# Kernel optimization log

Measured on AMD Instinct MI355X. Metric: run time of the kernel, lower is better.

The kernel has to match this reference:

```python
import jax, jax.numpy as jnp
import numpy as np

B, S, DIM = 2, 2048, 2048
N_HEADS, N_KV_HEADS = 16, 4
HEAD_DIM = DIM // N_HEADS  # 128
N_REP = N_HEADS // N_KV_HEADS
ROPE_THETA = 10000.0


def _rope_cos_sin(bsz, seqlen, head_dim, theta):
    # precompute_freqs_cis (unscaled): angles[t, i] = t * theta^{-2i/d}
    inv_freq = 1.0 / (theta ** (np.arange(0, head_dim, 2)[: head_dim // 2].astype(np.float32) / head_dim))
    t = np.arange(seqlen, dtype=np.float32)
    ang = np.outer(t, inv_freq)  # [S, hd/2]
    cos = np.broadcast_to(np.cos(ang), (bsz, seqlen, head_dim // 2))
    sin = np.broadcast_to(np.sin(ang), (bsz, seqlen, head_dim // 2))
    return jnp.asarray(cos), jnp.asarray(sin)


def setup_inputs() -> dict:
    key = jax.random.key(0)
    ks = jax.random.split(key, 5)
    scale = 1.0 / np.sqrt(DIM)
    x = jax.random.normal(ks[0], (B, S, DIM), dtype=jnp.float32)
    wq = jax.random.normal(ks[1], (DIM, N_HEADS * HEAD_DIM), dtype=jnp.float32) * scale
    wk = jax.random.normal(ks[2], (DIM, N_KV_HEADS * HEAD_DIM), dtype=jnp.float32) * scale
    wv = jax.random.normal(ks[3], (DIM, N_KV_HEADS * HEAD_DIM), dtype=jnp.float32) * scale
    wo = jax.random.normal(ks[4], (N_HEADS * HEAD_DIM, DIM), dtype=jnp.float32) * scale
    freqs_cos, freqs_sin = _rope_cos_sin(B, S, HEAD_DIM, ROPE_THETA)
    return {"x": x, "wq": wq, "wk": wk, "wv": wv, "wo": wo,
            "freqs_cos": freqs_cos, "freqs_sin": freqs_sin}


def _apply_rope(t, cos, sin):
    # t: [B, S, H, hd]; cos/sin: [B, S, hd/2] -> complex mult on (even, odd) pairs
    tr = t.reshape(*t.shape[:-1], -1, 2)  # [B,S,H,hd/2,2]
    xr, xi = tr[..., 0], tr[..., 1]
    c = cos[:, :, None, :]
    s = sin[:, :, None, :]
    out_r = xr * c - xi * s
    out_i = xr * s + xi * c
    return jnp.stack([out_r, out_i], axis=-1).reshape(t.shape)


def reference(x, wq, wk, wv, wo, freqs_cos, freqs_sin):
    bsz, seqlen, _ = x.shape
    xq = (x @ wq).reshape(bsz, seqlen, N_HEADS, HEAD_DIM)
    xk = (x @ wk).reshape(bsz, seqlen, N_KV_HEADS, HEAD_DIM)
    xv = (x @ wv).reshape(bsz, seqlen, N_KV_HEADS, HEAD_DIM)

    xq = _apply_rope(xq, freqs_cos, freqs_sin)
    xk = _apply_rope(xk, freqs_cos, freqs_sin)

    # repeat_kv (GQA): [B,S,KV,hd] -> [B,S,H,hd]
    xk = jnp.repeat(xk, N_REP, axis=2)
    xv = jnp.repeat(xv, N_REP, axis=2)

    # [B,H,Sq,Sk]
    scores = jnp.einsum('bqhd,bkhd->bhqk', xq, xk) / np.sqrt(HEAD_DIM).astype(np.float32)
    # additive causal mask (triu of -inf, diagonal=1)
    causal = jnp.triu(jnp.full((seqlen, seqlen), -jnp.inf, dtype=scores.dtype), k=1)
    scores = scores + causal
    probs = jax.nn.softmax(scores.astype(jnp.float32), axis=-1).astype(xq.dtype)
    out = jnp.einsum('bhqk,bkhd->bqhd', probs, xv).reshape(bsz, seqlen, -1)
    return out @ wo
```

## Files before the change

kernel.cpp:

```cpp
#include <hip/hip_runtime.h>
#include <stdint.h>

#define SEQ   2048
#define NB    2
#define LDQKV 3072
#define HD    128
#define QSCALE2 (0.08838834764831845f * 1.44269504088896340f)

typedef __attribute__((ext_vector_type(8))) short short8;
typedef __attribute__((ext_vector_type(4))) short short4v;
typedef __attribute__((ext_vector_type(4))) float f32x4;
typedef __attribute__((ext_vector_type(16))) float f32x16;
typedef __attribute__((ext_vector_type(4))) unsigned int u32x4;
typedef __attribute__((ext_vector_type(2))) unsigned int u32x2;
typedef __attribute__((ext_vector_type(8))) __bf16 bf16x8;

__device__ __forceinline__ float bs2f(short s) {
  unsigned int u = ((unsigned int)(unsigned short)s) << 16;
  return __builtin_bit_cast(float, u);
}
__device__ __forceinline__ short f2bs(float f) {
  unsigned int u = __builtin_bit_cast(unsigned int, f);
  u += 0x7fffu + ((u >> 16) & 1u);
  return (short)(u >> 16);
}
__device__ __forceinline__ unsigned int cvt_pk(float lo, float hi) {
  unsigned int r;
  asm("v_cvt_pk_bf16_f32 %0, %1, %2" : "=v"(r) : "v"(lo), "v"(hi));
  return r;
}
__device__ __forceinline__ f32x4 mfma16(short8 a, short8 b, f32x4 c) {
  return __builtin_amdgcn_mfma_f32_16x16x32_bf16(
      __builtin_bit_cast(bf16x8, a), __builtin_bit_cast(bf16x8, b), c, 0, 0, 0);
}
__device__ __forceinline__ f32x16 mfma32(short8 a, short8 b, f32x16 c) {
  return __builtin_amdgcn_mfma_f32_32x32x16_bf16(
      __builtin_bit_cast(bf16x8, a), __builtin_bit_cast(bf16x8, b), c, 0, 0, 0);
}
__device__ __forceinline__ void gload_lds16(const void* g, void* l) {
  __builtin_amdgcn_global_load_lds(
      (__attribute__((address_space(1))) const void*)(uintptr_t)g,
      (__attribute__((address_space(3))) void*)(unsigned int)(uintptr_t)l,
      16, 0, 0);
}

#define SBAR() asm volatile("s_barrier" ::: "memory")
#define VMC(n) asm volatile("s_waitcnt vmcnt(" #n ")" ::: "memory")

__global__ __launch_bounds__(256) void k_prep(const float* __restrict__ x,
                                              const float* __restrict__ wq,
                                              const float* __restrict__ wk,
                                              const float* __restrict__ wv,
                                              const float* __restrict__ wo,
                                              short* __restrict__ xb,
                                              short* __restrict__ wT,
                                              short* __restrict__ woT) {
  __shared__ __align__(16) float tile[64][68];
  const int bid = blockIdx.x, t = threadIdx.x;
  if (bid < 4096) {
    int i = bid * 256 + t;
    f32x4 a = *(const f32x4*)(x + (size_t)i * 8);
    f32x4 b = *(const f32x4*)(x + (size_t)i * 8 + 4);
    short8 o;
#pragma unroll
    for (int j = 0; j < 4; ++j) { o[j] = f2bs(a[j]); o[4 + j] = f2bs(b[j]); }
    *(short8*)(xb + (size_t)i * 8) = o;
    return;
  }
  const float* src;
  short* dst;
  int N, id;
  if (bid < 5120)      { id = bid - 4096; src = wq; dst = wT;                        N = 2048; }
  else if (bid < 5376) { id = bid - 5120; src = wk; dst = wT + (size_t)2048 * 2048;  N = 512;  }
  else if (bid < 5632) { id = bid - 5376; src = wv; dst = wT + (size_t)2560 * 2048;  N = 512;  }
  else                 { id = bid - 5632; src = wo; dst = woT;                       N = 2048; }
  const int K = 2048;
  int k0 = (id & 31) * 64, n0 = (id >> 5) * 64;
#pragma unroll
  for (int rep = 0; rep < 4; ++rep) {
    int lin = rep * 1024 + t * 4;
    int kk = lin >> 6, nn = lin & 63;
    f32x4 v = *(const f32x4*)(src + (size_t)(k0 + kk) * N + n0 + nn);
    *(f32x4*)(&tile[kk][nn]) = v;
  }
  __syncthreads();
#pragma unroll
  for (int rep = 0; rep < 4; ++rep) {
    int lin = rep * 1024 + t * 4;
    int nn = lin >> 6, kk = lin & 63;
    short4v o;
#pragma unroll
    for (int j = 0; j < 4; ++j) o[j] = f2bs(tile[kk + j][nn]);
    *(short4v*)(dst + (size_t)(n0 + nn) * K + k0 + kk) = o;
  }
}

template <int NH, int FP32OUT>
__global__ __launch_bounds__(512, 2) void k_gemm256(const short* __restrict__ A,
                                                    const short* __restrict__ Bt,
                                                    void* __restrict__ Cp,
                                                    int M, int N, int K) {
  __shared__ short Al[2][2][128 * 64];
  __shared__ short Bl[2][NH][128 * 64];
  const int t = threadIdx.x, l = t & 63, w = t >> 6;
  const int pm = w >> 2, pn = w & 3;
  const int lrow = l & 15, lg = l >> 4;
  const int NT = K >> 6;

  const int nbm = M >> 8;
  const int per = gridDim.x >> 3;
  const int id2 = (blockIdx.x & 7) * per + (blockIdx.x >> 3);
  const int m0 = (id2 % nbm) * 256, n0 = (id2 / nbm) * (NH * 128);

  const int srow = w * 8 + (l >> 3);
  const int sgx = ((l & 7) ^ (srow & 7)) * 8;
  const short* Abase = A + (size_t)(m0 + srow) * K + sgx;
  const short* Bbase = Bt + (size_t)(n0 + srow) * K + sgx;

  f32x4 acc[8][NH * 2] = {};
  short8 aFr0[4][2], aFr1[4][2], bFr[NH][2][2];

  auto stgA = [&](int d, int h, int tv) {
    const short* g = Abase + (size_t)(h * 128) * K + (size_t)tv * 64;
    gload_lds16(g, &Al[d][h][w * 512]);
    gload_lds16(g + (size_t)64 * K, &Al[d][h][w * 512 + 4096]);
  };
  auto stgB = [&](int d, int h, int tv) {
    const short* g = Bbase + (size_t)(h * 128) * K + (size_t)tv * 64;
    gload_lds16(g, &Bl[d][h][w * 512]);
    gload_lds16(g + (size_t)64 * K, &Bl[d][h][w * 512 + 4096]);
  };
  auto rdA = [&](int d, int Mh, short8 (*dst)[2]) {
#pragma unroll
    for (int mi = 0; mi < 4; ++mi) {
      int rl = pm * 64 + mi * 16 + lrow;
#pragma unroll
      for (int kk = 0; kk < 2; ++kk)
        dst[mi][kk] = *(const short8*)&Al[d][Mh][rl * 64 +
                                                 (((kk * 4 + lg) ^ (rl & 7)) * 8)];
    }
  };
  auto rdB = [&](int d) {
#pragma unroll
    for (int h = 0; h < NH; ++h)
#pragma unroll
      for (int ni = 0; ni < 2; ++ni) {
        int rl = pn * 32 + ni * 16 + lrow;
#pragma unroll
        for (int kk = 0; kk < 2; ++kk)
          bFr[h][ni][kk] =
              *(const short8*)&Bl[d][h][rl * 64 +
                                        (((kk * 4 + lg) ^ (rl & 7)) * 8)];
      }
  };

#define MMH(Mh, FR)                                                          \
  do {                                                                       \
    __builtin_amdgcn_s_setprio(1);                                           \
    _Pragma("unroll") for (int h = 0; h < NH; ++h)                           \
        _Pragma("unroll") for (int mi = 0; mi < 4; ++mi)                     \
            _Pragma("unroll") for (int ni = 0; ni < 2; ++ni)                 \
                _Pragma("unroll") for (int kk = 0; kk < 2; ++kk)             \
                    acc[(Mh)*4 + mi][h * 2 + ni] =                           \
                        mfma16(FR[mi][kk], bFr[h][ni][kk],                   \
                               acc[(Mh)*4 + mi][h * 2 + ni]);                \
    __builtin_amdgcn_s_setprio(0);                                           \
  } while (0)

  stgA(0, 0, 0);
  for (int h = 0; h < NH; ++h) stgB(0, h, 0);
  stgA(0, 1, 0);
  stgA(1, 0, 1);
  if (NH == 2) stgB(1, 1, 1);
  if (NH == 2) { VMC(4); } else { VMC(2); }
  SBAR();

  for (int v = 0; v < NT; ++v) {
    const int d = v & 1, d1 = d ^ 1;
    rdA(d, 0, aFr0);
    rdB(d);
    rdA(d, 1, aFr1);
    if (v + 1 < NT) { stgB(d1, 0, v + 1); stgA(d1, 1, v + 1); }
    MMH(0, aFr0);
    SBAR();
    if (v + 2 < NT) {
      stgA(d, 0, v + 2);
      if (NH == 2) stgB(d, 1, v + 2);
    }
    MMH(1, aFr1);
    if (v + 2 < NT) {
      if (NH == 2) { VMC(4); } else { VMC(2); }
    } else {
      VMC(0);
    }
    SBAR();
  }
#undef MMH

#pragma unroll
  for (int Mh = 0; Mh < 2; ++Mh)
#pragma unroll
    for (int mi = 0; mi < 4; ++mi)
#pragma unroll
      for (int h = 0; h < NH; ++h)
#pragma unroll
        for (int ni = 0; ni < 2; ++ni) {
          int row = m0 + Mh * 128 + pm * 64 + mi * 16 + lg * 4;
          int col = n0 + h * 128 + pn * 32 + ni * 16 + lrow;
          f32x4 vv = acc[Mh * 4 + mi][h * 2 + ni];
#pragma unroll
          for (int v2 = 0; v2 < 4; ++v2) {
            if constexpr (FP32OUT)
              ((float*)Cp)[(size_t)(row + v2) * N + col] = vv[v2];
            else
              ((short*)Cp)[(size_t)(row + v2) * N + col] = f2bs(vv[v2]);
          }
        }
}

__global__ __launch_bounds__(256) void k_rv(short* __restrict__ qkv,
                                            const float* __restrict__ fcos,
                                            const float* __restrict__ fsin,
                                            short* __restrict__ vt) {
  __shared__ short tile[128 * 137];
  const int bid = blockIdx.x, t = threadIdx.x;
  if (bid < 5120) {
    int tid = bid * 256 + t;
    int p16 = tid & 15;
    int slice = (tid >> 4) % 20;
    int bs = tid / 320;
    int col = (slice < 16) ? slice * 128 + p16 * 8
                           : 2048 + (slice - 16) * 128 + p16 * 8;
    short8 x = *(short8*)(qkv + (size_t)bs * LDQKV + col);
    f32x4 c = *(const f32x4*)(fcos + (size_t)bs * 64 + p16 * 4);
    f32x4 s = *(const f32x4*)(fsin + (size_t)bs * 64 + p16 * 4);
    float sc = (slice < 16) ? QSCALE2 : 1.0f;
    short8 o;
#pragma unroll
    for (int j = 0; j < 4; ++j) {
      float xr = bs2f(x[2 * j]), xi = bs2f(x[2 * j + 1]);
      o[2 * j] = f2bs((xr * c[j] - xi * s[j]) * sc);
      o[2 * j + 1] = f2bs((xr * s[j] + xi * c[j]) * sc);
    }
    *(short8*)(qkv + (size_t)bs * LDQKV + col) = o;
    return;
  }
  const int id = bid - 5120;
  int s0 = (id & 15) * 128;
  int kvh = (id >> 4) & 3, b = id >> 6;
  const short* src = qkv + (size_t)(b * SEQ) * LDQKV + 2560 + kvh * 128;
#pragma unroll
  for (int rep = 0; rep < 8; ++rep) {
    int lin = rep * 2048 + t * 8;
    int si = lin >> 7, d = lin & 127;
    short8 v = *(const short8*)(src + (size_t)(s0 + si) * LDQKV + d);
#pragma unroll
    for (int j = 0; j < 8; ++j) tile[si * 137 + d + j] = v[j];
  }
  __syncthreads();
  short* dst = vt + (size_t)((b * 4 + kvh) * 128) * SEQ;
#pragma unroll
  for (int rep = 0; rep < 8; ++rep) {
    int lin = rep * 2048 + t * 8;
    int d = lin >> 7, sb = lin & 127;
    short8 o;
#pragma unroll
    for (int j = 0; j < 8; ++j) o[j] = tile[(sb + j) * 137 + d];
    *(short8*)(dst + (size_t)d * SEQ + s0 + sb) = o;
  }
}

__global__ __launch_bounds__(256, 2) void k_attn(const short* __restrict__ qkv,
                                                 const short* __restrict__ vt,
                                                 short* __restrict__ outp) {
  __shared__ short Ks[2][64 * 128];
  __shared__ short Vs[2][128 * 64];
  const int t = threadIdx.x, l = t & 63, w = t >> 6;
  const int wr = w >> 1, wk = w & 1;
  const int h = blockIdx.y, b = blockIdx.z;
  const int kvh = h >> 2;
  const int lo5 = l & 31, hi = l >> 5;

  const int kkey = t >> 4, kd8 = t & 15;
  const int vdd = t >> 3, vs8 = t & 7;
  const short* kbase = qkv + (size_t)(b * SEQ) * LDQKV + 2048 + kvh * HD;
  const short* vbase = vt + (size_t)((b * 4 + kvh) * 128) * SEQ;

  auto stageKV = [&](int buf, int it) {
    const int kt = it * 64;
    short* kdst = &Ks[buf][w * 512];
    short* vdst = &Vs[buf][w * 512];
#pragma unroll
    for (int i = 0; i < 4; ++i) {
      int key = i * 16 + kkey;
      int sd = (kd8 ^ (key & 15)) * 8;
      gload_lds16(kbase + (size_t)(kt + key) * LDQKV + sd, kdst + i * 2048);
    }
#pragma unroll
    for (int i = 0; i < 4; ++i) {
      int d = i * 32 + vdd;
      int ss = (vs8 ^ (d & 7)) * 8;
      gload_lds16(vbase + (size_t)d * SEQ + kt + ss, vdst + i * 2048);
    }
  };

  int koff[8], voff[4][2];
#pragma unroll
  for (int s = 0; s < 8; ++s)
    koff[s] = (wk * 32 + lo5) * 128 + (((hi + 2 * s) ^ (l & 15)) * 8);
#pragma unroll
  for (int db = 0; db < 4; ++db)
#pragma unroll
    for (int s = 0; s < 2; ++s)
      voff[db][s] =
          (db * 32 + lo5) * 64 + (((4 * wk + hi + 2 * s) ^ (l & 7)) * 8);
  const int kbloc = wk * 32 + 4 * hi;
  const int qloc = wr * 32 + lo5;

  for (int part = 0; part < 2; ++part) {
    const int qt = part ? (31 - (int)blockIdx.x) : (int)blockIdx.x;
    const int q0 = qt * 64;

    short8 qf[8];
    {
      const short* qrow =
          qkv + (size_t)(b * SEQ + q0 + wr * 32 + lo5) * LDQKV + h * HD;
#pragma unroll
      for (int s = 0; s < 8; ++s)
        qf[s] = *(const short8*)(qrow + s * 16 + hi * 8);
    }

    f32x16 of[4] = {};
    float mrun = 0.f, lsum = 0.f;

    const int nt = qt + 1;
    stageKV(0, 0);
    __syncthreads();

    for (int it = 0; it < nt; ++it) {
      const int buf = it & 1;
      if (it + 1 < nt) stageKV(buf ^ 1, it + 1);
      const short* KsC = Ks[buf];
      const short* VsC = Vs[buf];

      f32x16 sc = {};
      __builtin_amdgcn_s_setprio(1);
#pragma unroll
      for (int s = 0; s < 8; ++s) {
        short8 kf = *(const short8*)(KsC + koff[s]);
        sc = mfma32(kf, qf[s], sc);
      }
      __builtin_amdgcn_s_setprio(0);

      if (it == nt - 1) {
#pragma unroll
        for (int r = 0; r < 16; ++r) {
          const int off = (r & 3) + 8 * (r >> 2);
          if (kbloc + off > qloc) sc[r] = -1e30f;
        }
      }

      float lmax = sc[0];
#pragma unroll
      for (int r = 1; r < 16; ++r) lmax = fmaxf(lmax, sc[r]);
      if (__any(lmax > mrun + 8.f)) {
        float mx = fmaxf(lmax, __shfl_xor(lmax, 32));
        float mm = fmaxf(mrun, mx);
        float rs = exp2f(mrun - mm);
        mrun = mm;
        lsum *= rs;
#pragma unroll
        for (int db = 0; db < 4; ++db)
#pragma unroll
          for (int r = 0; r < 16; ++r) of[db][r] *= rs;
      }

      float p[16];
#pragma unroll
      for (int r = 0; r < 16; ++r) {
        p[r] = exp2f(sc[r] - mrun);
        lsum += p[r];
      }
      unsigned int pk[8];
#pragma unroll
      for (int j = 0; j < 8; ++j) pk[j] = cvt_pk(p[2 * j], p[2 * j + 1]);

      unsigned int s0 = hi ? pk[0] : pk[2];
      unsigned int s1 = hi ? pk[1] : pk[3];
      unsigned int s2 = hi ? pk[4] : pk[6];
      unsigned int s3 = hi ? pk[5] : pk[7];
      unsigned int x0 = __shfl_xor(s0, 32);
      unsigned int x1 = __shfl_xor(s1, 32);
      unsigned int x2 = __shfl_xor(s2, 32);
      unsigned int x3 = __shfl_xor(s3, 32);
      u32x4 b0w, b1w;
      b0w.x = hi ? x0 : pk[0];
      b0w.y = hi ? x1 : pk[1];
      b0w.z = hi ? pk[2] : x0;
      b0w.w = hi ? pk[3] : x1;
      b1w.x = hi ? x2 : pk[4];
      b1w.y = hi ? x3 : pk[5];
      b1w.z = hi ? pk[6] : x2;
      b1w.w = hi ? pk[7] : x3;
      short8 pb[2] = {__builtin_bit_cast(short8, b0w),
                      __builtin_bit_cast(short8, b1w)};

      __builtin_amdgcn_s_setprio(1);
#pragma unroll
      for (int s = 0; s < 2; ++s)
#pragma unroll
        for (int db = 0; db < 4; ++db) {
          short8 vf = *(const short8*)(VsC + voff[db][s]);
          of[db] = mfma32(vf, pb[s], of[db]);
        }
      __builtin_amdgcn_s_setprio(0);
      __syncthreads();
    }

    lsum += __shfl_xor(lsum, 32);
    float* og = (float*)Ks;
    float* sg = (float*)Vs;
    if (wk == 1) {
#pragma unroll
      for (int db = 0; db < 4; ++db)
#pragma unroll
        for (int r4 = 0; r4 < 4; ++r4) {
          int g = db * 4 + r4;
          f32x4 v;
#pragma unroll
          for (int j = 0; j < 4; ++j) v[j] = of[db][r4 * 4 + j];
          *(f32x4*)&og[wr * 4096 + l * 64 + ((g ^ (l & 15)) * 4)] = v;
        }
      sg[wr * 64 + l] = mrun;
      sg[128 + wr * 64 + l] = lsum;
    }
    __syncthreads();
    if (wk == 0) {
      float m1 = sg[wr * 64 + l];
      float l1 = sg[128 + wr * 64 + l];
      float mt = fmaxf(mrun, m1);
      float r0 = exp2f(mrun - mt), r1 = exp2f(m1 - mt);
      float inv = 1.0f / (lsum * r0 + l1 * r1);
      short* ob =
          outp + (size_t)(b * SEQ + q0 + wr * 32 + lo5) * 2048 + h * HD;
#pragma unroll
      for (int db = 0; db < 4; ++db) {
#pragma unroll
        for (int r4 = 0; r4 < 4; ++r4) {
          int g = db * 4 + r4;
          f32x4 o1 = *(const f32x4*)&og[wr * 4096 + l * 64 +
                                        ((g ^ (l & 15)) * 4)];
          u32x2 pko;
          float v0 = (of[db][r4 * 4 + 0] * r0 + o1[0] * r1) * inv;
          float v1 = (of[db][r4 * 4 + 1] * r0 + o1[1] * r1) * inv;
          float v2 = (of[db][r4 * 4 + 2] * r0 + o1[2] * r1) * inv;
          float v3 = (of[db][r4 * 4 + 3] * r0 + o1[3] * r1) * inv;
          pko.x = cvt_pk(v0, v1);
          pko.y = cvt_pk(v2, v3);
          *(u32x2*)(ob + db * 32 + 8 * r4 + 4 * hi) = pko;
        }
      }
    }
    __syncthreads();
  }
}

extern "C" void kernel_launch(void* const* d_in, const int* in_sizes, int n_in,
                              void* d_out, int out_size, void* d_ws,
                              size_t ws_size, hipStream_t stream) {
  const float* x = (const float*)d_in[0];
  const float* wq = (const float*)d_in[1];
  const float* wk = (const float*)d_in[2];
  const float* wv = (const float*)d_in[3];
  const float* wo = (const float*)d_in[4];
  const float* fc = (const float*)d_in[5];
  const float* fs = (const float*)d_in[6];

  char* ws = (char*)d_ws;
  short* xb = (short*)(ws);
  short* wT = (short*)(ws + (16ull << 20));
  short* woT = (short*)(ws + (28ull << 20));
  short* qkvb = (short*)(ws + (36ull << 20));
  short* vtb = (short*)(ws + (16ull << 20));
  short* attn = (short*)(ws);

  k_prep<<<6656, 256, 0, stream>>>(x, wq, wk, wv, wo, xb, wT, woT);
  k_gemm256<2, 0><<<192, 512, 0, stream>>>(xb, wT, qkvb, 4096, 3072, 2048);
  k_rv<<<5248, 256, 0, stream>>>(qkvb, fc, fs, vtb);
  k_attn<<<dim3(16, 16, 2), 256, 0, stream>>>(qkvb, vtb, attn);
  k_gemm256<1, 1><<<256, 512, 0, stream>>>(attn, woT, d_out, 4096, 2048, 2048);
}
```

Measured before the change: 189.9 us.

## Fuse RoPE into QKV GEMM epilogue, split QK MFMA chain, use raw v_exp

Moves the RoPE rotation and Q scaling out of the separate k_rv pass and into the QKV GEMM epilogue, pairing even and odd columns through a lane shuffle, so the extra read-modify-write of Q and K in qkv is gone. The leftover kernel only transposes V. In attention, the QK^T MFMA accumulation is split into two independent chains to cut dependency latency, and exp2f is replaced by the raw v_exp_f32 instruction. This risks slight numerical differences: RoPE now runs on fp32 accumulators before bf16 rounding, and v_exp skips denormal handling.

```diff
diff --git a/kernel.cpp b/kernel.cpp
--- a/kernel.cpp
+++ b/kernel.cpp
@@ -27,6 +27,11 @@
 __device__ __forceinline__ unsigned int cvt_pk(float lo, float hi) {
   unsigned int r;
   asm("v_cvt_pk_bf16_f32 %0, %1, %2" : "=v"(r) : "v"(lo), "v"(hi));
+  return r;
+}
+__device__ __forceinline__ float fexp2(float x) {
+  float r;
+  asm("v_exp_f32 %0, %1" : "=v"(r) : "v"(x));
   return r;
 }
 __device__ __forceinline__ f32x4 mfma16(short8 a, short8 b, f32x4 c) {
@@ -95,10 +100,12 @@
   }
 }
 
-template <int NH, int FP32OUT>
+template <int NH, int FP32OUT, int ROPE>
 __global__ __launch_bounds__(512, 2) void k_gemm256(const short* __restrict__ A,
                                                     const short* __restrict__ Bt,
                                                     void* __restrict__ Cp,
+                                                    const float* __restrict__ fcos,
+                                                    const float* __restrict__ fsin,
                                                     int M, int N, int K) {
   __shared__ short Al[2][2][128 * 64];
   __shared__ short Bl[2][NH][128 * 64];
@@ -208,6 +215,21 @@
           int row = m0 + Mh * 128 + pm * 64 + mi * 16 + lg * 4;
           int col = n0 + h * 128 + pn * 32 + ni * 16 + lrow;
           f32x4 vv = acc[Mh * 4 + mi][h * 2 + ni];
+          if constexpr (ROPE) {
+            if (col < 2560) {
+              const float qs = (col < 2048) ? QSCALE2 : 1.0f;
+              const int p = (col & 127) >> 1;
+              const bool ev = ((lrow & 1) == 0);
+#pragma unroll
+              for (int v2 = 0; v2 < 4; ++v2) {
+                float c = fcos[(size_t)(row + v2) * 64 + p] * qs;
+                float s = fsin[(size_t)(row + v2) * 64 + p] * qs;
+                float xx = vv[v2];
+                float xp = __shfl_xor(xx, 1);
+                vv[v2] = ev ? (xx * c - xp * s) : (xp * s + xx * c);
+              }
+            }
+          }
 #pragma unroll
           for (int v2 = 0; v2 < 4; ++v2) {
             if constexpr (FP32OUT)
@@ -218,34 +240,10 @@
         }
 }
 
-__global__ __launch_bounds__(256) void k_rv(short* __restrict__ qkv,
-                                            const float* __restrict__ fcos,
-                                            const float* __restrict__ fsin,
+__global__ __launch_bounds__(256) void k_vt(const short* __restrict__ qkv,
                                             short* __restrict__ vt) {
   __shared__ short tile[128 * 137];
-  const int bid = blockIdx.x, t = threadIdx.x;
-  if (bid < 5120) {
-    int tid = bid * 256 + t;
-    int p16 = tid & 15;
-    int slice = (tid >> 4) % 20;
-    int bs = tid / 320;
-    int col = (slice < 16) ? slice * 128 + p16 * 8
-                           : 2048 + (slice - 16) * 128 + p16 * 8;
-    short8 x = *(short8*)(qkv + (size_t)bs * LDQKV + col);
-    f32x4 c = *(const f32x4*)(fcos + (size_t)bs * 64 + p16 * 4);
-    f32x4 s = *(const f32x4*)(fsin + (size_t)bs * 64 + p16 * 4);
-    float sc = (slice < 16) ? QSCALE2 : 1.0f;
-    short8 o;
-#pragma unroll
-    for (int j = 0; j < 4; ++j) {
-      float xr = bs2f(x[2 * j]), xi = bs2f(x[2 * j + 1]);
-      o[2 * j] = f2bs((xr * c[j] - xi * s[j]) * sc);
-      o[2 * j + 1] = f2bs((xr * s[j] + xi * c[j]) * sc);
-    }
-    *(short8*)(qkv + (size_t)bs * LDQKV + col) = o;
-    return;
-  }
-  const int id = bid - 5120;
+  const int id = blockIdx.x, t = threadIdx.x;
   int s0 = (id & 15) * 128;
   int kvh = (id >> 4) & 3, b = id >> 6;
   const short* src = qkv + (size_t)(b * SEQ) * LDQKV + 2560 + kvh * 128;
@@ -343,14 +341,17 @@
       const short* KsC = Ks[buf];
       const short* VsC = Vs[buf];
 
-      f32x16 sc = {};
+      f32x16 sca = {}, scb = {};
       __builtin_amdgcn_s_setprio(1);
 #pragma unroll
-      for (int s = 0; s < 8; ++s) {
-        short8 kf = *(const short8*)(KsC + koff[s]);
-        sc = mfma32(kf, qf[s], sc);
+      for (int s = 0; s < 4; ++s) {
+        short8 kf0 = *(const short8*)(KsC + koff[2 * s]);
+        short8 kf1 = *(const short8*)(KsC + koff[2 * s + 1]);
+        sca = mfma32(kf0, qf[2 * s], sca);
+        scb = mfma32(kf1, qf[2 * s + 1], scb);
       }
       __builtin_amdgcn_s_setprio(0);
+      f32x16 sc = sca + scb;
 
       if (it == nt - 1) {
 #pragma unroll
@@ -366,7 +367,7 @@
       if (__any(lmax > mrun + 8.f)) {
         float mx = fmaxf(lmax, __shfl_xor(lmax, 32));
         float mm = fmaxf(mrun, mx);
-        float rs = exp2f(mrun - mm);
+        float rs = fexp2(mrun - mm);
         mrun = mm;
         lsum *= rs;
 #pragma unroll
@@ -378,7 +379,7 @@
       float p[16];
 #pragma unroll
       for (int r = 0; r < 16; ++r) {
-        p[r] = exp2f(sc[r] - mrun);
+        p[r] = fexp2(sc[r] - mrun);
         lsum += p[r];
       }
       unsigned int pk[8];
@@ -439,7 +440,7 @@
       float m1 = sg[wr * 64 + l];
       float l1 = sg[128 + wr * 64 + l];
       float mt = fmaxf(mrun, m1);
-      float r0 = exp2f(mrun - mt), r1 = exp2f(m1 - mt);
+      float r0 = fexp2(mrun - mt), r1 = fexp2(m1 - mt);
       float inv = 1.0f / (lsum * r0 + l1 * r1);
       short* ob =
           outp + (size_t)(b * SEQ + q0 + wr * 32 + lo5) * 2048 + h * HD;
@@ -485,8 +486,10 @@
   short* attn = (short*)(ws);
 
   k_prep<<<6656, 256, 0, stream>>>(x, wq, wk, wv, wo, xb, wT, woT);
-  k_gemm256<2, 0><<<192, 512, 0, stream>>>(xb, wT, qkvb, 4096, 3072, 2048);
-  k_rv<<<5248, 256, 0, stream>>>(qkvb, fc, fs, vtb);
+  k_gemm256<2, 0, 1><<<192, 512, 0, stream>>>(xb, wT, qkvb, fc, fs,
+                                              4096, 3072, 2048);
+  k_vt<<<128, 256, 0, stream>>>(qkvb, vtb);
   k_attn<<<dim3(16, 16, 2), 256, 0, stream>>>(qkvb, vtb, attn);
-  k_gemm256<1, 1><<<256, 512, 0, stream>>>(attn, woT, d_out, 4096, 2048, 2048);
-}
+  k_gemm256<1, 1, 0><<<256, 512, 0, stream>>>(attn, woT, d_out, nullptr,
+                                              nullptr, 4096, 2048, 2048);
+}
```

New measurement: 183.1 us. 1.04x faster.
